# Optimization experiments

Hardware: AMD Instinct MI355X
Metric: run time of the kernel (lower is better)

The kernel has to match this reference:

```python
import jax, jax.numpy as jnp
import numpy as np

EPS = 1e-5  # torch BatchNorm default eps


def bn_silu(h, g, b, m, v):
    # eval-mode BatchNorm followed by SiLU (spnn.BatchNorm + spnn.SiLU on node features)
    return jax.nn.silu((h - m) * jax.lax.rsqrt(v + EPS) * g + b)


def sparse_conv(h, idx, valid, W, bias):
    # submanifold sparse conv as gather + per-offset matmul + accumulate
    # h: [N, Ci], idx/valid: [K, N], W: [K, Ci, Co]
    g = h[idx] * valid[..., None].astype(h.dtype)  # [K, N, Ci]
    return jnp.einsum('knc,kcf->nf', g, W) + bias


def setup_inputs() -> dict:
    key = jax.random.key(0)
    ks = jax.random.split(key, 16)
    N, C, B, NE, K = 100000, 64, 16, 256, 27
    x = jax.random.normal(ks[0], (N, C), jnp.float32)
    t = jax.random.normal(ks[1], (B, NE), jnp.float32)
    b = jnp.sort(jax.random.randint(ks[2], (N,), 0, B)).astype(jnp.int32)
    kmap_idx = jax.random.randint(ks[3], (K, N), 0, N).astype(jnp.int32)
    kmap_valid = (jax.random.uniform(ks[4], (K, N)) < 0.5).astype(jnp.int32)
    # center offset is the node itself and always present
    kmap_idx = kmap_idx.at[K // 2].set(jnp.arange(N, dtype=jnp.int32))
    kmap_valid = kmap_valid.at[K // 2].set(1)

    def nrm(k, shape, s=1.0):
        return jax.random.normal(k, shape, jnp.float32) * s

    return {
        'x': x, 't': t, 'b': b, 'kmap_idx': kmap_idx, 'kmap_valid': kmap_valid,
        'bn1_g': 1.0 + nrm(ks[5], (C,), 0.1), 'bn1_b': nrm(ks[6], (C,), 0.1),
        'bn1_m': nrm(ks[7], (C,), 0.1), 'bn1_v': jax.random.uniform(ks[8], (C,)) + 0.5,
        'W1': nrm(ks[9], (K, C, C), 0.02), 'b1c': nrm(ks[10], (C,), 0.02),
        'bn2_g': 1.0 + nrm(ks[11], (C,), 0.1), 'bn2_b': nrm(ks[12], (C,), 0.1),
        'bn2_m': nrm(ks[13], (C,), 0.1), 'bn2_v': jax.random.uniform(ks[14], (C,)) + 0.5,
        'W2': nrm(ks[15], (K, C, C), 0.02), 'b2c': nrm(jax.random.fold_in(key, 100), (C,), 0.02),
        'Wt': nrm(jax.random.fold_in(key, 101), (NE, 2 * C), 0.05),
        'bt': nrm(jax.random.fold_in(key, 102), (2 * C,), 0.02),
    }


def reference(x, t, b, kmap_idx, kmap_valid,
              bn1_g, bn1_b, bn1_m, bn1_v, W1, b1c,
              bn2_g, bn2_b, bn2_m, bn2_v, W2, b2c,
              Wt, bt):
    # conv1 = BN -> SiLU -> sparse Conv3d
    h = sparse_conv(bn_silu(x, bn1_g, bn1_b, bn1_m, bn1_v), kmap_idx, kmap_valid, W1, b1c)
    # TimeEmbeddingBlock: per-batch FiLM, gathered per node via batch index b
    tp = jax.nn.silu(t) @ Wt + bt              # [B, 2*nf]
    scale, shift = jnp.split(tp, 2, axis=-1)   # [B, nf] each
    h = (1.0 + scale[b]) * h + shift[b]
    # conv2 = BN -> SiLU -> sparse Conv3d
    h = sparse_conv(bn_silu(h, bn2_g, bn2_b, bn2_m, bn2_v), kmap_idx, kmap_valid, W2, b2c)
    # residual; ni == nf so idconv is identity (fc.noop)
    return h + x
```

## Files before the change

### kernel.cpp

```cpp
#include <hip/hip_runtime.h>

typedef __attribute__((ext_vector_type(16))) float f32x16;
typedef __attribute__((ext_vector_type(2))) long lv2;
typedef __attribute__((ext_vector_type(2))) unsigned int uint2v;

#define BN_EPS 1e-5f
#define KOFF 27
#define LSTRIDE 72

static __device__ __forceinline__ float silu_f(float z) {
  return z / (1.f + __expf(-z));
}

static __device__ __forceinline__ unsigned char f2fp8(float v) {
  unsigned int p = (unsigned int)__builtin_amdgcn_cvt_pk_fp8_f32(v, 0.f, 0, 0);
  return (unsigned char)(p & 0xffu);
}

__global__ void prep_all(const float* __restrict__ t, const float* __restrict__ Wt,
                         const float* __restrict__ bt,
                         float* __restrict__ scale_eff, float* __restrict__ shift,
                         const float* __restrict__ W1, const float* __restrict__ W2,
                         unsigned char* __restrict__ Wp1, unsigned char* __restrict__ Wp2,
                         const float* __restrict__ x, const float* __restrict__ g1,
                         const float* __restrict__ b1, const float* __restrict__ m1,
                         const float* __restrict__ v1, unsigned char* __restrict__ a1,
                         int total) {
  const int bid = blockIdx.x;
  if (bid < 864) {
    int tid = bid * 256 + threadIdx.x;
    const int tot = KOFF * 8 * 64 * 8;
    const float* W = W1;
    unsigned char* Wp = Wp1;
    if (tid >= tot) { tid -= tot; W = W2; Wp = Wp2; }
    int j = tid & 7, lane = (tid >> 3) & 63, f = (tid >> 9) & 7, k = tid >> 12;
    int ci = (f >> 1) * 16 + (lane >> 5) * 8 + j;
    int co = (f & 1) * 32 + (lane & 31);
    Wp[tid] = f2fp8(W[(k * 64 + ci) * 64 + co]);
  } else if (bid < 872) {
    int tid = (bid - 864) * 256 + threadIdx.x;
    int bi = tid >> 7, co = tid & 127;
    float acc = bt[co];
    for (int e = 0; e < 256; ++e) {
      float tv = t[bi * 256 + e];
      acc += silu_f(tv) * Wt[e * 128 + co];
    }
    if (co < 64) scale_eff[bi * 64 + co] = 1.f + acc;
    else         shift[bi * 64 + (co - 64)] = acc;
  } else {
    int i = ((bid - 872) * 256 + threadIdx.x) * 8;
    if (i >= total) {
      if (i < total + 64) *(uint2v*)(a1 + i) = (uint2v){0u, 0u};
      return;
    }
    float4 va = *(const float4*)(x + i);
    float4 vb = *(const float4*)(x + i + 4);
    int c = i & 63;
    float4 ga = *(const float4*)(g1 + c), gb = *(const float4*)(g1 + c + 4);
    float4 ba = *(const float4*)(b1 + c), bbv = *(const float4*)(b1 + c + 4);
    float4 ma = *(const float4*)(m1 + c), mb = *(const float4*)(m1 + c + 4);
    float4 vva = *(const float4*)(v1 + c), vvb = *(const float4*)(v1 + c + 4);
    float z0 = silu_f((va.x - ma.x) * (ga.x * rsqrtf(vva.x + BN_EPS)) + ba.x);
    float z1 = silu_f((va.y - ma.y) * (ga.y * rsqrtf(vva.y + BN_EPS)) + ba.y);
    float z2 = silu_f((va.z - ma.z) * (ga.z * rsqrtf(vva.z + BN_EPS)) + ba.z);
    float z3 = silu_f((va.w - ma.w) * (ga.w * rsqrtf(vva.w + BN_EPS)) + ba.w);
    float z4 = silu_f((vb.x - mb.x) * (gb.x * rsqrtf(vvb.x + BN_EPS)) + bbv.x);
    float z5 = silu_f((vb.y - mb.y) * (gb.y * rsqrtf(vvb.y + BN_EPS)) + bbv.y);
    float z6 = silu_f((vb.z - mb.z) * (gb.z * rsqrtf(vvb.z + BN_EPS)) + bbv.z);
    float z7 = silu_f((vb.w - mb.w) * (gb.w * rsqrtf(vvb.w + BN_EPS)) + bbv.w);
    unsigned int w0 = (unsigned int)__builtin_amdgcn_cvt_pk_fp8_f32(z0, z1, 0, 0);
    w0 = (unsigned int)__builtin_amdgcn_cvt_pk_fp8_f32(z2, z3, (int)w0, 1);
    unsigned int w1 = (unsigned int)__builtin_amdgcn_cvt_pk_fp8_f32(z4, z5, 0, 0);
    w1 = (unsigned int)__builtin_amdgcn_cvt_pk_fp8_f32(z6, z7, (int)w1, 1);
    *(uint2v*)(a1 + i) = (uint2v){w0, w1};
  }
}

template <int MODE>
__global__ __launch_bounds__(256, 6) void conv_k(
    const unsigned char* __restrict__ act, const int* __restrict__ idx,
    const int* __restrict__ valid,
    const unsigned char* __restrict__ Wp,
    const float* __restrict__ bias,
    const float* __restrict__ scale_eff, const float* __restrict__ shift,
    const int* __restrict__ bidx,
    const float* __restrict__ g2, const float* __restrict__ b2,
    const float* __restrict__ m2, const float* __restrict__ v2,
    const float* __restrict__ xres,
    unsigned char* __restrict__ out8, float* __restrict__ out_f, int N) {
  __shared__ unsigned char ldsA[2][64 * LSTRIDE];
  __shared__ unsigned char ldsW[2][4096];
  __shared__ int rI[3][2][64];
  __shared__ int rV[3][2][64];

  if (MODE == 0 && blockIdx.x == 0 && threadIdx.x < 64) {
    out8[(size_t)N * 64 + threadIdx.x] = 0;
  }
  const int tid = threadIdx.x;
  const int lane = tid & 63;
  const int wid = tid >> 6;
  const int half = lane >> 5;
  const int r32 = lane & 31;
  const int n0 = blockIdx.x * 64;

  const int q0 = lane & 3;
  const int rL = wid * 16 + (lane >> 2);
  const int nS = min(n0 + rL, N - 1);
  const int RH = wid >> 1;
  const int cb = wid & 1;

  f32x16 acc;
#pragma unroll
  for (int i = 0; i < 16; ++i) acc[i] = 0.f;

  lv2 st0, st1, st2;
  lv2 wstA, wstB;
  int gr = 0;

#define GRPLOAD(g) do { \
    int tp = min(2 * (g) + (q0 >> 1), KOFF - 1); \
    const int* bp = (q0 & 1) ? valid : idx; \
    gr = bp[(size_t)tp * N + nS]; \
  } while (0)

#define RINGWRITE(g) do { \
    int* p = (q0 & 1) ? &rV[(g) % 3][q0 >> 1][rL] : &rI[(g) % 3][q0 >> 1][rL]; \
    *p = gr; \
  } while (0)

#define RINGREAD(t) \
    (rV[((t) >> 1) % 3][(t) & 1][rL] ? rI[((t) >> 1) % 3][(t) & 1][rL] : N)

#define GLOAD(st, rv) do { \
    st = *(const lv2*)(act + (size_t)(rv) * 64 + q0 * 16); \
  } while (0)

#define WGLOAD(kk, wst) do { \
    wst = *(const lv2*)(Wp + (size_t)(kk) * 4096 + tid * 16); \
  } while (0)

#define DSWRITE(buf, st) do { \
    unsigned char* _p = &ldsA[buf][rL * LSTRIDE + q0 * 16]; \
    *(long*)_p = st.x; \
    *(long*)(_p + 8) = st.y; \
  } while (0)

#define DSWRITE_W(buf, wst) do { \
    unsigned char* _p = &ldsW[buf][tid * 16]; \
    *(long*)_p = wst.x; \
    *(long*)(_p + 8) = wst.y; \
  } while (0)

#define COMPUTE(buf) do { \
    _Pragma("unroll") \
    for (int ks = 0; ks < 4; ++ks) { \
      long av = *(const long*)(&ldsA[buf][(RH * 32 + r32) * LSTRIDE + ks * 16 + half * 8]); \
      long wv = *(const long*)(&ldsW[buf][((ks * 2 + cb) * 64 + lane) * 8]); \
      acc = __builtin_amdgcn_mfma_f32_32x32x16_fp8_fp8(av, wv, acc, 0, 0, 0); \
    } } while (0)

#define BARRIER() do { \
    asm volatile("s_waitcnt lgkmcnt(0)" ::: "memory"); \
    __builtin_amdgcn_s_barrier(); \
  } while (0)

  GRPLOAD(0); RINGWRITE(0);
  GRPLOAD(1); RINGWRITE(1);
  GRPLOAD(2); RINGWRITE(2);
  BARRIER();
  {
    int rv0 = RINGREAD(0);
    GLOAD(st0, rv0);
    int rv1 = RINGREAD(1);
    GLOAD(st1, rv1);
    int rv2 = RINGREAD(2);
    GLOAD(st2, rv2);
  }
  WGLOAD(0, wstA);
  WGLOAD(1, wstB);
  DSWRITE(0, st0);
  DSWRITE_W(0, wstA);
  BARRIER();

#pragma unroll
  for (int k = 0; k < KOFF; ++k) {
    if (k + 1 < KOFF) {
      const int s = (k + 1) % 3;
      if (s == 0)      DSWRITE((k + 1) & 1, st0);
      else if (s == 1) DSWRITE((k + 1) & 1, st1);
      else             DSWRITE((k + 1) & 1, st2);
      if ((k + 1) & 1) DSWRITE_W(1, wstB); else DSWRITE_W(0, wstA);
    }
    if (!(k & 1) && k <= 20) GRPLOAD((k + 6) / 2);
    if ((k & 1) && k <= 21)  RINGWRITE((k + 5) / 2);
    if (k + 2 < KOFF) {
      if (k & 1) WGLOAD(k + 2, wstB); else WGLOAD(k + 2, wstA);
    }
    if (k + 3 < KOFF) {
      int rv = RINGREAD(k + 3);
      const int s = (k + 3) % 3;
      if (s == 0)      GLOAD(st0, rv);
      else if (s == 1) GLOAD(st1, rv);
      else             GLOAD(st2, rv);
    }
    COMPUTE(k & 1);
    if (k + 1 < KOFF) BARRIER();
  }
#undef GRPLOAD
#undef RINGWRITE
#undef RINGREAD
#undef GLOAD
#undef WGLOAD
#undef DSWRITE
#undef DSWRITE_W
#undef COMPUTE
#undef BARRIER

  if (MODE == 0) {
    const int c = cb * 32 + r32;
    float bb = bias[c];
    float s2v = g2[c] * rsqrtf(v2[c] + BN_EPS);
    float o2v = b2[c] - m2[c] * s2v;
#pragma unroll
    for (int r = 0; r < 16; ++r) {
      int rowD = (r & 3) + 8 * (r >> 2) + 4 * half;
      int n = n0 + RH * 32 + rowD;
      if (n < N) {
        int bi = bidx[n];
        float h = acc[r] + bb;
        h = scale_eff[bi * 64 + c] * h + shift[bi * 64 + c];
        float z = h * s2v + o2v;
        out8[(size_t)n * 64 + c] = f2fp8(silu_f(z));
      }
    }
  } else {
    const int c = cb * 32 + r32;
    float bb = bias[c];
#pragma unroll
    for (int r = 0; r < 16; ++r) {
      int rowD = (r & 3) + 8 * (r >> 2) + 4 * half;
      int n = n0 + RH * 32 + rowD;
      if (n < N) {
        out_f[(size_t)n * 64 + c] = acc[r] + bb + xres[(size_t)n * 64 + c];
      }
    }
  }
}

extern "C" void kernel_launch(void* const* d_in, const int* in_sizes, int n_in,
                              void* d_out, int out_size, void* d_ws, size_t ws_size,
                              hipStream_t stream) {
  const float* x    = (const float*)d_in[0];
  const float* t    = (const float*)d_in[1];
  const int*   b    = (const int*)d_in[2];
  const int*   kidx = (const int*)d_in[3];
  const int*   kval = (const int*)d_in[4];
  const float* bn1g = (const float*)d_in[5];
  const float* bn1b = (const float*)d_in[6];
  const float* bn1m = (const float*)d_in[7];
  const float* bn1v = (const float*)d_in[8];
  const float* W1   = (const float*)d_in[9];
  const float* b1c  = (const float*)d_in[10];
  const float* bn2g = (const float*)d_in[11];
  const float* bn2b = (const float*)d_in[12];
  const float* bn2m = (const float*)d_in[13];
  const float* bn2v = (const float*)d_in[14];
  const float* W2   = (const float*)d_in[15];
  const float* b2c  = (const float*)d_in[16];
  const float* Wt   = (const float*)d_in[17];
  const float* bt   = (const float*)d_in[18];
  float* out = (float*)d_out;

  const int N = in_sizes[2];
  const int total = N * 64;

  char* ws = (char*)d_ws;
  size_t actB = ((size_t)(N + 1) * 64 + 255) & ~(size_t)255;
  unsigned char* a1 = (unsigned char*)ws;
  unsigned char* a2 = (unsigned char*)(ws + actB);
  const size_t wpackB = (size_t)KOFF * 8 * 64 * 8;
  unsigned char* W1p = (unsigned char*)(ws + 2 * actB);
  unsigned char* W2p = (unsigned char*)(ws + 2 * actB + wpackB);
  float* scale_eff = (float*)(ws + 2 * actB + 2 * wpackB);
  float* shiftp    = scale_eff + 16 * 64;

  int bnblk = (total / 8 + 8 + 255) / 256;
  prep_all<<<872 + bnblk, 256, 0, stream>>>(t, Wt, bt, scale_eff, shiftp,
                                            W1, W2, W1p, W2p,
                                            x, bn1g, bn1b, bn1m, bn1v, a1, total);

  int nblk = (N + 63) / 64;
  conv_k<0><<<nblk, 256, 0, stream>>>(a1, kidx, kval, W1p, b1c, scale_eff,
                                      shiftp, b, bn2g, bn2b, bn2m, bn2v,
                                      nullptr, a2, nullptr, N);
  conv_k<1><<<nblk, 256, 0, stream>>>(a2, kidx, kval, W2p, b2c, nullptr, nullptr,
                                      nullptr, nullptr, nullptr, nullptr, nullptr,
                                      x, nullptr, out, N);
}
```

Baseline: 100.1 us.

## Pack kernel-map validity into per-node bitmask and restructure index ring

Adds a prep stage that packs the 27 per-offset valid flags into one 32-bit mask per node, so both conv kernels read one word per node instead of 27 valid ints each. The index ring in LDS now holds only indices, four offsets per group, which shrinks shared memory and the prefetch schedule. Weight packing is rewritten to stage each offset through a shared tile and store 16 bytes per thread instead of byte-wise scattered writes. Launch bounds are raised to 8 waves per SIMD, which risks register spills.

```diff
diff --git a/kernel.cpp b/kernel.cpp
--- a/kernel.cpp
+++ b/kernel.cpp
@@ -17,29 +17,44 @@
   return (unsigned char)(p & 0xffu);
 }
 
-__global__ void prep_all(const float* __restrict__ t, const float* __restrict__ Wt,
+__global__ void prep_all(int vblk,
+                         const float* __restrict__ t, const float* __restrict__ Wt,
                          const float* __restrict__ bt,
                          float* __restrict__ scale_eff, float* __restrict__ shift,
                          const float* __restrict__ W1, const float* __restrict__ W2,
                          unsigned char* __restrict__ Wp1, unsigned char* __restrict__ Wp2,
+                         const int* __restrict__ kval, unsigned int* __restrict__ vmask,
                          const float* __restrict__ x, const float* __restrict__ g1,
                          const float* __restrict__ b1, const float* __restrict__ m1,
                          const float* __restrict__ v1, unsigned char* __restrict__ a1,
-                         int total) {
+                         int N, int total) {
+  __shared__ float tile[4096];
   const int bid = blockIdx.x;
-  if (bid < 864) {
-    int tid = bid * 256 + threadIdx.x;
-    const int tot = KOFF * 8 * 64 * 8;
-    const float* W = W1;
-    unsigned char* Wp = Wp1;
-    if (tid >= tot) { tid -= tot; W = W2; Wp = Wp2; }
-    int j = tid & 7, lane = (tid >> 3) & 63, f = (tid >> 9) & 7, k = tid >> 12;
-    int ci = (f >> 1) * 16 + (lane >> 5) * 8 + j;
-    int co = (f & 1) * 32 + (lane & 31);
-    Wp[tid] = f2fp8(W[(k * 64 + ci) * 64 + co]);
-  } else if (bid < 872) {
-    int tid = (bid - 864) * 256 + threadIdx.x;
-    int bi = tid >> 7, co = tid & 127;
+  const int tid = threadIdx.x;
+  if (bid < 54) {
+    int which = bid >= KOFF;
+    int k = bid - which * KOFF;
+    const float* Wk = (which ? W2 : W1) + (size_t)k * 4096;
+    unsigned char* Wp = (which ? Wp2 : Wp1) + (size_t)k * 4096;
+#pragma unroll
+    for (int j = 0; j < 16; ++j) tile[j * 256 + tid] = Wk[j * 256 + tid];
+    __syncthreads();
+    int f = tid >> 5;
+    int lane0 = (tid & 31) * 2;
+    alignas(16) unsigned char obuf[16];
+#pragma unroll
+    for (int li = 0; li < 2; ++li) {
+      int lane = lane0 + li;
+      int cib = (f >> 1) * 16 + (lane >> 5) * 8;
+      int co = (f & 1) * 32 + (lane & 31);
+#pragma unroll
+      for (int j = 0; j < 8; ++j)
+        obuf[li * 8 + j] = f2fp8(tile[(cib + j) * 64 + co]);
+    }
+    *(lv2*)(Wp + tid * 16) = *(const lv2*)obuf;
+  } else if (bid < 62) {
+    int id = (bid - 54) * 256 + tid;
+    int bi = id >> 7, co = id & 127;
     float acc = bt[co];
     for (int e = 0; e < 256; ++e) {
       float tv = t[bi * 256 + e];
@@ -47,8 +62,17 @@
     }
     if (co < 64) scale_eff[bi * 64 + co] = 1.f + acc;
     else         shift[bi * 64 + (co - 64)] = acc;
+  } else if (bid < 62 + vblk) {
+    int n = (bid - 62) * 256 + tid;
+    if (n < N) {
+      unsigned int u = 0;
+#pragma unroll
+      for (int k = 0; k < KOFF; ++k)
+        u |= (kval[(size_t)k * N + n] ? 1u : 0u) << k;
+      vmask[n] = u;
+    }
   } else {
-    int i = ((bid - 872) * 256 + threadIdx.x) * 8;
+    int i = ((bid - 62 - vblk) * 256 + tid) * 8;
     if (i >= total) {
       if (i < total + 64) *(uint2v*)(a1 + i) = (uint2v){0u, 0u};
       return;
@@ -77,9 +101,9 @@
 }
 
 template <int MODE>
-__global__ __launch_bounds__(256, 6) void conv_k(
+__global__ __launch_bounds__(256, 8) void conv_k(
     const unsigned char* __restrict__ act, const int* __restrict__ idx,
-    const int* __restrict__ valid,
+    const unsigned int* __restrict__ vmask,
     const unsigned char* __restrict__ Wp,
     const float* __restrict__ bias,
     const float* __restrict__ scale_eff, const float* __restrict__ shift,
@@ -90,8 +114,7 @@
     unsigned char* __restrict__ out8, float* __restrict__ out_f, int N) {
   __shared__ unsigned char ldsA[2][64 * LSTRIDE];
   __shared__ unsigned char ldsW[2][4096];
-  __shared__ int rI[3][2][64];
-  __shared__ int rV[3][2][64];
+  __shared__ int rI[2][4][64];
 
   if (MODE == 0 && blockIdx.x == 0 && threadIdx.x < 64) {
     out8[(size_t)N * 64 + threadIdx.x] = 0;
@@ -116,20 +139,17 @@
   lv2 st0, st1, st2;
   lv2 wstA, wstB;
   int gr = 0;
+  const unsigned int vm = vmask[nS];
 
 #define GRPLOAD(g) do { \
-    int tp = min(2 * (g) + (q0 >> 1), KOFF - 1); \
-    const int* bp = (q0 & 1) ? valid : idx; \
-    gr = bp[(size_t)tp * N + nS]; \
-  } while (0)
-
-#define RINGWRITE(g) do { \
-    int* p = (q0 & 1) ? &rV[(g) % 3][q0 >> 1][rL] : &rI[(g) % 3][q0 >> 1][rL]; \
-    *p = gr; \
-  } while (0)
+    int tp = min(4 * (g) + q0, KOFF - 1); \
+    gr = idx[(size_t)tp * N + nS]; \
+  } while (0)
+
+#define RINGWRITE(g) do { rI[(g) & 1][q0][rL] = gr; } while (0)
 
 #define RINGREAD(t) \
-    (rV[((t) >> 1) % 3][(t) & 1][rL] ? rI[((t) >> 1) % 3][(t) & 1][rL] : N)
+    (((vm >> (t)) & 1u) ? rI[((t) >> 2) & 1][(t) & 3][rL] : N)
 
 #define GLOAD(st, rv) do { \
     st = *(const lv2*)(act + (size_t)(rv) * 64 + q0 * 16); \
@@ -166,7 +186,6 @@
 
   GRPLOAD(0); RINGWRITE(0);
   GRPLOAD(1); RINGWRITE(1);
-  GRPLOAD(2); RINGWRITE(2);
   BARRIER();
   {
     int rv0 = RINGREAD(0);
@@ -191,8 +210,8 @@
       else             DSWRITE((k + 1) & 1, st2);
       if ((k + 1) & 1) DSWRITE_W(1, wstB); else DSWRITE_W(0, wstA);
     }
-    if (!(k & 1) && k <= 20) GRPLOAD((k + 6) / 2);
-    if ((k & 1) && k <= 21)  RINGWRITE((k + 5) / 2);
+    if (!(k & 3) && k <= 16)      GRPLOAD(k / 4 + 2);
+    if ((k & 3) == 2 && k <= 18)  RINGWRITE(k / 4 + 2);
     if (k + 2 < KOFF) {
       if (k & 1) WGLOAD(k + 2, wstB); else WGLOAD(k + 2, wstA);
     }
@@ -283,17 +302,20 @@
   unsigned char* W2p = (unsigned char*)(ws + 2 * actB + wpackB);
   float* scale_eff = (float*)(ws + 2 * actB + 2 * wpackB);
   float* shiftp    = scale_eff + 16 * 64;
-
+  unsigned int* vmask = (unsigned int*)(ws + 2 * actB + 2 * wpackB + 8192);
+
+  int vblk = (N + 255) / 256;
   int bnblk = (total / 8 + 8 + 255) / 256;
-  prep_all<<<872 + bnblk, 256, 0, stream>>>(t, Wt, bt, scale_eff, shiftp,
-                                            W1, W2, W1p, W2p,
-                                            x, bn1g, bn1b, bn1m, bn1v, a1, total);
+  prep_all<<<62 + vblk + bnblk, 256, 0, stream>>>(vblk, t, Wt, bt, scale_eff, shiftp,
+                                                  W1, W2, W1p, W2p, kval, vmask,
+                                                  x, bn1g, bn1b, bn1m, bn1v, a1,
+                                                  N, total);
 
   int nblk = (N + 63) / 64;
-  conv_k<0><<<nblk, 256, 0, stream>>>(a1, kidx, kval, W1p, b1c, scale_eff,
+  conv_k<0><<<nblk, 256, 0, stream>>>(a1, kidx, vmask, W1p, b1c, scale_eff,
                                       shiftp, b, bn2g, bn2b, bn2m, bn2v,
                                       nullptr, a2, nullptr, N);
-  conv_k<1><<<nblk, 256, 0, stream>>>(a2, kidx, kval, W2p, b2c, nullptr, nullptr,
+  conv_k<1><<<nblk, 256, 0, stream>>>(a2, kidx, vmask, W2p, b2c, nullptr, nullptr,
                                       nullptr, nullptr, nullptr, nullptr, nullptr,
                                       x, nullptr, out, N);
 }
```

After: 100.8 us, median of 2. Within noise of the previous version (+0.7%).
